# Optimization experiments

Hardware: AMD Instinct MI355X
Metric: run time of the kernel (lower is better)

Reference implementation:

```python
import jax, jax.numpy as jnp
import numpy as np

D_MODEL = 1024
N_HEADS = 16
D_HEAD = D_MODEL // N_HEADS
D_FF = 4096
B, T = 2, 2048


def layer_norm(x, gamma, beta, eps=1e-5):
    mu = jnp.mean(x, axis=-1, keepdims=True)
    var = jnp.var(x, axis=-1, keepdims=True)
    return (x - mu) * jax.lax.rsqrt(var + eps) * gamma + beta


def setup_inputs() -> dict:
    key = jax.random.key(0)
    ks = jax.random.split(key, 8)
    s = D_MODEL ** -0.5
    return {
        "x": jax.random.normal(ks[0], (B, T, D_MODEL), dtype=jnp.float32),
        "w_qkv": jax.random.normal(ks[1], (D_MODEL, 3 * D_MODEL), dtype=jnp.float32) * s,
        "w_out": jax.random.normal(ks[2], (D_MODEL, D_MODEL), dtype=jnp.float32) * s,
        "ln1_g": jnp.ones((D_MODEL,), jnp.float32),
        "ln1_b": jnp.zeros((D_MODEL,), jnp.float32),
        "ln2_g": jnp.ones((D_MODEL,), jnp.float32),
        "ln2_b": jnp.zeros((D_MODEL,), jnp.float32),
        "w1": jax.random.normal(ks[3], (D_MODEL, D_FF), dtype=jnp.float32) * s,
        "b1": jnp.zeros((D_FF,), jnp.float32),
        "w2": jax.random.normal(ks[4], (D_FF, D_MODEL), dtype=jnp.float32) * (D_FF ** -0.5),
        "b2": jnp.zeros((D_MODEL,), jnp.float32),
    }


def reference(x, w_qkv, w_out, ln1_g, ln1_b, ln2_g, ln2_b, w1, b1, w2, b2):
    Bb, Tt, C = x.shape
    h = layer_norm(x, ln1_g, ln1_b)
    qkv = h @ w_qkv  # [B,T,3C]
    q, k, v = jnp.split(qkv, 3, axis=-1)

    def heads(t):  # [B,T,C] -> [B,H,T,Dh]
        return t.reshape(Bb, Tt, N_HEADS, D_HEAD).transpose(0, 2, 1, 3)

    q, k, v = heads(q), heads(k), heads(v)
    scale = D_HEAD ** -0.5
    attn = jnp.einsum("bhqd,bhkd->bhqk", q, k) * scale
    causal = jnp.tril(jnp.ones((Tt, Tt), dtype=bool))
    attn = jnp.where(causal[None, None], attn, -jnp.inf)
    attn = jax.nn.softmax(attn, axis=-1)
    out = jnp.einsum("bhqk,bhkd->bhqd", attn, v)
    out = out.transpose(0, 2, 1, 3).reshape(Bb, Tt, C)
    x = x + out @ w_out
    h2 = layer_norm(x, ln2_g, ln2_b)
    ff = jax.nn.gelu(h2 @ w1 + b1, approximate=False) @ w2 + b2
    return x + ff
```

## Files before the change

### kernel.cpp

```cpp
#include <hip/hip_runtime.h>
#include <hip/hip_bf16.h>
#include <cstdint>

#define DM 1024
#define DFF 4096
#define NB 2
#define TT 2048
#define NH 16
#define DH 64

typedef unsigned short u16;
typedef __bf16 bf16x8 __attribute__((ext_vector_type(8)));
typedef float f32x4 __attribute__((ext_vector_type(4)));

__device__ __forceinline__ u16 f2b(float f) {
    union { float f; unsigned u; } v; v.f = f;
    unsigned u = v.u;
    return (u16)((u + 0x7FFFu + ((u >> 16) & 1u)) >> 16);
}

__device__ __forceinline__ unsigned cvtpk(float a, float b) {
    unsigned r;
    asm("v_cvt_pk_bf16_f32 %0, %1, %2" : "=v"(r) : "v"(a), "v"(b));
    return r;
}

__device__ __forceinline__ float gelu_fast(float z) {
    const float u = z * z;
    const float w = z * __builtin_fmaf(u, 0.10294324f, 2.3022082f);
    const float e = exp2f(w);
    const float r = __builtin_amdgcn_rcpf(1.0f + e);
    return z - z * r;
}

__device__ __forceinline__ f32x4 mfma_bf16(bf16x8 a, bf16x8 b, f32x4 c) {
    return __builtin_amdgcn_mfma_f32_16x16x32_bf16(a, b, c, 0, 0, 0);
}

__device__ __forceinline__ void gload_lds16(const void* g, void* l) {
    __builtin_amdgcn_global_load_lds((const __attribute__((address_space(1))) unsigned int*)g,
                                     (__attribute__((address_space(3))) unsigned int*)l, 16, 0, 0);
}

__global__ __launch_bounds__(256) void transW(const float* __restrict__ W, u16* __restrict__ Wt,
                                              int K, int N) {
    __shared__ float t[32][33];
    int tx = threadIdx.x & 31, ty = threadIdx.x >> 5;
    int k0 = blockIdx.y * 32, n0 = blockIdx.x * 32;
#pragma unroll
    for (int j = 0; j < 4; ++j)
        t[ty + 8 * j][tx] = W[(size_t)(k0 + ty + 8 * j) * N + n0 + tx];
    __syncthreads();
#pragma unroll
    for (int j = 0; j < 4; ++j)
        Wt[(size_t)(n0 + ty + 8 * j) * K + k0 + tx] = f2b(t[tx][ty + 8 * j]);
}

__global__ __launch_bounds__(256) void ln_kernel(const float* __restrict__ X,
                                                 const float* __restrict__ g,
                                                 const float* __restrict__ bt,
                                                 u16* __restrict__ H) {
    int row = blockIdx.x, tid = threadIdx.x;
    float4 v = ((const float4*)(X + (size_t)row * DM))[tid];
    float s = v.x + v.y + v.z + v.w;
    float ss = v.x * v.x + v.y * v.y + v.z * v.z + v.w * v.w;
#pragma unroll
    for (int off = 32; off >= 1; off >>= 1) {
        s += __shfl_xor(s, off);
        ss += __shfl_xor(ss, off);
    }
    __shared__ float sb[8];
    int w = tid >> 6, lane = tid & 63;
    if (lane == 0) { sb[w] = s; sb[4 + w] = ss; }
    __syncthreads();
    s = sb[0] + sb[1] + sb[2] + sb[3];
    ss = sb[4] + sb[5] + sb[6] + sb[7];
    float mu = s * (1.0f / DM);
    float var = ss * (1.0f / DM) - mu * mu;
    float rstd = rsqrtf(var + 1e-5f);
    float4 gv = ((const float4*)g)[tid];
    float4 bv = ((const float4*)bt)[tid];
    uint2 hv;
    hv.x = cvtpk((v.x - mu) * rstd * gv.x + bv.x, (v.y - mu) * rstd * gv.y + bv.y);
    hv.y = cvtpk((v.z - mu) * rstd * gv.z + bv.z, (v.w - mu) * rstd * gv.w + bv.w);
    ((uint2*)(H + (size_t)row * DM))[tid] = hv;
}

__global__ __launch_bounds__(256) void add_kernel(float* __restrict__ out,
                                                  const float* __restrict__ part, int n4) {
    int idx = blockIdx.x * 256 + threadIdx.x;
    const int stride = gridDim.x * 256;
    for (; idx < n4; idx += stride) {
        float4 a = ((const float4*)out)[idx];
        float4 p = ((const float4*)part)[idx];
        a.x += p.x; a.y += p.y; a.z += p.z; a.w += p.w;
        ((float4*)out)[idx] = a;
    }
}

template <int MODE, int DBUF, int SPLIT>
__global__ __launch_bounds__(256) void gemm_kernel(
    const u16* __restrict__ A, const u16* __restrict__ Bt, int M, int N, int K,
    u16* __restrict__ oq, u16* __restrict__ ok, u16* __restrict__ vt,
    const float* __restrict__ resid, float* __restrict__ outf,
    const float* __restrict__ bias, u16* __restrict__ outbf,
    float* __restrict__ part) {
    __shared__ __align__(16) u16 Alds[DBUF + 1][128][64];
    __shared__ __align__(16) u16 Blds[DBUF + 1][128][64];
    const int tid = threadIdx.x;
    const int lane = tid & 63;
    const int w = tid >> 6;
    const int wr = w >> 1, wc = w & 1;
    int bid = blockIdx.x + gridDim.x * blockIdx.y;
    const int nwg = gridDim.x * gridDim.y;
    bid = (bid & 7) * (nwg >> 3) + (bid >> 3);
    int mrow = bid / gridDim.x;
    int ks = 0;
    if constexpr (SPLIT) {
        const int mtiles = (nwg / gridDim.x) >> 1;
        ks = mrow >= mtiles;
        mrow -= ks * mtiles;
    }
    const int bm = mrow * 128, bn = (bid % gridDim.x) * 128;
    const int kbeg = SPLIT ? ks * (K >> 1) : 0;
    const int kend = SPLIT ? kbeg + (K >> 1) : K;
    const int l15 = lane & 15, lg = lane >> 4;
    const int srow = tid >> 3, pch = tid & 7;
    const int lc = pch ^ (srow & 7);

    f32x4 acc[4][4] = {};
    const u16* Ap = A + (size_t)(bm + srow) * K + lc * 8;
    const u16* Bp = Bt + (size_t)(bn + srow) * K + lc * 8;

#define STAGE(buf, k0)                                                          \
    {                                                                           \
        _Pragma("unroll") for (int i = 0; i < 4; ++i) {                         \
            gload_lds16(Ap + (size_t)(32 * i) * K + (k0), &Alds[buf][srow + 32 * i][pch * 8]); \
            gload_lds16(Bp + (size_t)(32 * i) * K + (k0), &Blds[buf][srow + 32 * i][pch * 8]); \
        }                                                                       \
    }

#define COMPUTE(buf)                                                            \
    {                                                                           \
        _Pragma("unroll") for (int kk = 0; kk < 2; ++kk) {                      \
            bf16x8 af[4], bfr[4];                                               \
            _Pragma("unroll") for (int f = 0; f < 4; ++f) {                     \
                const int ar = wr * 64 + f * 16 + l15;                          \
                const int br = wc * 64 + f * 16 + l15;                          \
                const int kch = kk * 4 + lg;                                    \
                af[f] = *(const bf16x8*)&Alds[buf][ar][(kch ^ (ar & 7)) * 8];   \
                bfr[f] = *(const bf16x8*)&Blds[buf][br][(kch ^ (br & 7)) * 8];  \
            }                                                                   \
            _Pragma("unroll") for (int mi = 0; mi < 4; ++mi)                    \
                _Pragma("unroll") for (int ni = 0; ni < 4; ++ni)                \
                    acc[mi][ni] = mfma_bf16(af[mi], bfr[ni], acc[mi][ni]);      \
        }                                                                       \
    }

    if constexpr (DBUF == 0) {
        for (int k0 = kbeg; k0 < kend; k0 += 64) {
            STAGE(0, k0);
            __syncthreads();
            COMPUTE(0);
            __syncthreads();
        }
    } else {
        STAGE(0, kbeg);
        for (int k0 = kbeg; k0 < kend; k0 += 64) {
            const int cur = ((k0 - kbeg) >> 6) & 1;
            if (k0 + 64 < kend) {
                STAGE(cur ^ 1, k0 + 64);
                asm volatile("s_waitcnt vmcnt(8)" ::: "memory");
            } else {
                asm volatile("s_waitcnt vmcnt(0)" ::: "memory");
            }
            __builtin_amdgcn_sched_barrier(0);
            __builtin_amdgcn_s_barrier();
            __builtin_amdgcn_sched_barrier(0);
            COMPUTE(cur);
            __builtin_amdgcn_s_barrier();
        }
    }
#undef STAGE
#undef COMPUTE

    const int m0 = bm + wr * 64, n0 = bn + wc * 64;
#pragma unroll
    for (int mi = 0; mi < 4; ++mi) {
#pragma unroll
        for (int ni = 0; ni < 4; ++ni) {
            if constexpr (MODE == 0) {
                const int n = n0 + ni * 16 + l15;
                const int which = n >> 10;
                const int hh = (n >> 6) & 15, d = n & 63;
                const int mbase = m0 + mi * 16 + 4 * lg;
                const int bb = mbase >> 11, t = mbase & 2047;
                if (which == 2) {
                    uint2 pv;
                    pv.x = cvtpk(acc[mi][ni][0], acc[mi][ni][1]);
                    pv.y = cvtpk(acc[mi][ni][2], acc[mi][ni][3]);
                    *(uint2*)(vt + (((size_t)(bb * NH + hh)) * DH + d) * TT + t) = pv;
                } else {
                    u16* dst = which == 0 ? oq : ok;
                    const float sc = which == 0 ? 0.18033688f : 1.0f;
                    const unsigned p01 = cvtpk(acc[mi][ni][0] * sc, acc[mi][ni][1] * sc);
                    const unsigned p23 = cvtpk(acc[mi][ni][2] * sc, acc[mi][ni][3] * sc);
                    u16* db = dst + (((size_t)(bb * NH + hh)) * TT + t) * DH + d;
                    db[0] = (u16)p01;
                    db[DH] = (u16)(p01 >> 16);
                    db[2 * DH] = (u16)p23;
                    db[3 * DH] = (u16)(p23 >> 16);
                }
            } else if constexpr (MODE == 2) {
                const int n = n0 + ni * 16 + l15;
                const float bn_ = bias[n];
                const float g0 = gelu_fast(acc[mi][ni][0] + bn_);
                const float g1 = gelu_fast(acc[mi][ni][1] + bn_);
                const float g2 = gelu_fast(acc[mi][ni][2] + bn_);
                const float g3 = gelu_fast(acc[mi][ni][3] + bn_);
                const unsigned p01 = cvtpk(g0, g1);
                const unsigned p23 = cvtpk(g2, g3);
                u16* db = outbf + (size_t)(m0 + mi * 16 + 4 * lg) * N + n;
                db[0] = (u16)p01;
                db[N] = (u16)(p01 >> 16);
                db[2 * N] = (u16)p23;
                db[3 * N] = (u16)(p23 >> 16);
            } else {
#pragma unroll
                for (int r = 0; r < 4; ++r) {
                    int m = m0 + mi * 16 + 4 * lg + r;
                    int n = n0 + ni * 16 + l15;
                    float v = acc[mi][ni][r];
                    size_t o = (size_t)m * N + n;
                    if constexpr (MODE == 1) {
                        outf[o] = resid[o] + v;
                    } else {
                        if (SPLIT && ks == 1)
                            part[o] = v;
                        else
                            outf[o] = resid[o] + v + bias[n];
                    }
                }
            }
        }
    }
}

__global__ __launch_bounds__(256) void attn_kernel(const u16* __restrict__ Q,
                                                   const u16* __restrict__ Kg,
                                                   const u16* __restrict__ Vtg,
                                                   u16* __restrict__ O) {
    __shared__ __align__(16) u16 Klds[4][64][64];
    __shared__ __align__(16) u16 Vlds[4][64][64];
    const int tid = threadIdx.x, lane = tid & 63, w = tid >> 6;
    const int l15 = lane & 15, lg = lane >> 4;

    int id = blockIdx.x + (blockIdx.y << 4);
    int sw = (id & 7) * 64 + (id >> 3);
    const int p = sw & 15, bh = sw >> 4;
    const size_t base = (size_t)bh * TT * DH;
    const int b = bh >> 4, hh = bh & 15;

    const int srow = tid >> 3, pch = tid & 7;
    const int lc = pch ^ (srow & 7);

    const int src0 = (((2 * lg) & 3) << 4) | l15;
    const int src1 = src0 + 16;
    const bool hi = (lg >> 1) != 0;

#define ASTAGE(buf, kv)                                                                     \
    {                                                                                       \
        gload_lds16(Kg + base + (size_t)((kv) * 64 + srow) * DH + lc * 8,                   \
                    &Klds[buf][srow][pch * 8]);                                             \
        gload_lds16(Kg + base + (size_t)((kv) * 64 + srow + 32) * DH + lc * 8,              \
                    &Klds[buf][srow + 32][pch * 8]);                                        \
        gload_lds16(Vtg + base + (size_t)srow * TT + (kv) * 64 + lc * 8,                    \
                    &Vlds[buf][srow][pch * 8]);                                             \
        gload_lds16(Vtg + base + (size_t)(srow + 32) * TT + (kv) * 64 + lc * 8,             \
                    &Vlds[buf][srow + 32][pch * 8]);                                        \
    }

    for (int half = 0; half < 2; ++half) {
        const int qt = half ? (31 - p) : p;
        const int nkv = qt + 1;
        const int qrow = qt * 64 + w * 16 + l15;
        uint4 qu0 = *(const uint4*)(Q + base + (size_t)qrow * DH + 8 * lg);
        uint4 qu1 = *(const uint4*)(Q + base + (size_t)qrow * DH + 32 + 8 * lg);
        asm volatile("" : "+v"(qu0.x), "+v"(qu0.y), "+v"(qu0.z), "+v"(qu0.w),
                          "+v"(qu1.x), "+v"(qu1.y), "+v"(qu1.z), "+v"(qu1.w));
        const bf16x8 qf0 = *(const bf16x8*)&qu0;
        const bf16x8 qf1 = *(const bf16x8*)&qu1;

        f32x4 o[4] = {};
        float lsum = 0.0f;

        auto compute_tile = [&](int buf, bool masked, int kvi) {
            f32x4 s[4] = {};
            __builtin_amdgcn_s_setprio(1);
#pragma unroll
            for (int nf = 0; nf < 4; ++nf) {
                const int row = nf * 16 + l15;
                bf16x8 kb0 = *(const bf16x8*)&Klds[buf][row][(lg ^ (l15 & 7)) * 8];
                bf16x8 kb1 = *(const bf16x8*)&Klds[buf][row][((4 + lg) ^ (l15 & 7)) * 8];
                s[nf] = mfma_bf16(kb0, qf0, s[nf]);
                s[nf] = mfma_bf16(kb1, qf1, s[nf]);
            }
            __builtin_amdgcn_s_setprio(0);

            if (masked) {
#pragma unroll
                for (int nf = 0; nf < 4; ++nf) {
                    const int tg = kvi * 64 + nf * 16 + 4 * lg;
#pragma unroll
                    for (int r = 0; r < 4; ++r)
                        if (tg + r > qrow) s[nf][r] = -1e30f;
                }
            }

            float ps = 0.0f;
#pragma unroll
            for (int nf = 0; nf < 4; ++nf) {
#pragma unroll
                for (int r = 0; r < 4; ++r) {
                    const float pp = exp2f(s[nf][r]);
                    s[nf][r] = pp;
                    ps += pp;
                }
            }
            lsum += ps;

            unsigned pk[4][2];
#pragma unroll
            for (int nf = 0; nf < 4; ++nf) {
                pk[nf][0] = cvtpk(s[nf][0], s[nf][1]);
                pk[nf][1] = cvtpk(s[nf][2], s[nf][3]);
            }
            bf16x8 pa[2];
#pragma unroll
            for (int kf = 0; kf < 2; ++kf) {
                unsigned a0 = __shfl((int)pk[2 * kf][0], src0);
                unsigned a1 = __shfl((int)pk[2 * kf][1], src0);
                unsigned a2 = __shfl((int)pk[2 * kf][0], src1);
                unsigned a3 = __shfl((int)pk[2 * kf][1], src1);
                unsigned c0 = __shfl((int)pk[2 * kf + 1][0], src0);
                unsigned c1 = __shfl((int)pk[2 * kf + 1][1], src0);
                unsigned c2 = __shfl((int)pk[2 * kf + 1][0], src1);
                unsigned c3 = __shfl((int)pk[2 * kf + 1][1], src1);
                uint4 wv;
                wv.x = hi ? c0 : a0;
                wv.y = hi ? c1 : a1;
                wv.z = hi ? c2 : a2;
                wv.w = hi ? c3 : a3;
                pa[kf] = *(const bf16x8*)&wv;
            }

            __builtin_amdgcn_s_setprio(1);
#pragma unroll
            for (int nf = 0; nf < 4; ++nf) {
                const int row = nf * 16 + l15;
                bf16x8 vb0 = *(const bf16x8*)&Vlds[buf][row][(lg ^ (l15 & 7)) * 8];
                bf16x8 vb1 = *(const bf16x8*)&Vlds[buf][row][((4 + lg) ^ (l15 & 7)) * 8];
                o[nf] = mfma_bf16(vb0, pa[0], o[nf]);
                o[nf] = mfma_bf16(vb1, pa[1], o[nf]);
            }
            __builtin_amdgcn_s_setprio(0);
        };

        ASTAGE(0, 0);
        if (nkv > 1) ASTAGE(1, 1);

        for (int kv = 0; kv < nkv; kv += 2) {
            int nst = 0;
            if (kv + 2 < nkv) { ASTAGE((kv + 2) & 3, kv + 2); nst += 4; }
            if (kv + 3 < nkv) { ASTAGE((kv + 3) & 3, kv + 3); nst += 4; }
            if (nst == 8)
                asm volatile("s_waitcnt vmcnt(8)" ::: "memory");
            else if (nst == 4)
                asm volatile("s_waitcnt vmcnt(4)" ::: "memory");
            else
                asm volatile("s_waitcnt vmcnt(0)" ::: "memory");
            __builtin_amdgcn_sched_barrier(0);
            __builtin_amdgcn_s_barrier();
            __builtin_amdgcn_sched_barrier(0);

            compute_tile(kv & 3, kv == qt, kv);
            if (kv + 1 < nkv) compute_tile((kv + 1) & 3, kv + 1 == qt, kv + 1);

            __builtin_amdgcn_s_barrier();
        }

        lsum += __shfl_xor(lsum, 16);
        lsum += __shfl_xor(lsum, 32);
        const float linv = 1.0f / lsum;
#pragma unroll
        for (int nf = 0; nf < 4; ++nf) {
            uint2 pv;
            pv.x = cvtpk(o[nf][0] * linv, o[nf][1] * linv);
            pv.y = cvtpk(o[nf][2] * linv, o[nf][3] * linv);
            *(uint2*)(O + ((size_t)b * TT + qrow) * DM + hh * DH + nf * 16 + 4 * lg) = pv;
        }
    }
#undef ASTAGE
}

extern "C" void kernel_launch(void* const* d_in, const int* in_sizes, int n_in,
                              void* d_out, int out_size, void* d_ws, size_t ws_size,
                              hipStream_t stream) {
    const float* x = (const float*)d_in[0];
    const float* wqkv = (const float*)d_in[1];
    const float* wout = (const float*)d_in[2];
    const float* ln1g = (const float*)d_in[3];
    const float* ln1b = (const float*)d_in[4];
    const float* ln2g = (const float*)d_in[5];
    const float* ln2b = (const float*)d_in[6];
    const float* w1 = (const float*)d_in[7];
    const float* b1 = (const float*)d_in[8];
    const float* w2 = (const float*)d_in[9];
    const float* b2 = (const float*)d_in[10];
    float* out = (float*)d_out;
    char* ws = (char*)d_ws;

    u16* wqkv_t = (u16*)(ws + 0);
    u16* wout_t = (u16*)(ws + 6291456);
    u16* w1_t   = (u16*)(ws + 8388608);
    u16* w2_t   = (u16*)(ws + 16777216);
    u16* h_bf   = (u16*)(ws + 25165824);
    u16* q_bf   = (u16*)(ws + 33554432);
    u16* k_bf   = (u16*)(ws + 41943040);
    u16* vt_bf  = (u16*)(ws + 50331648);
    u16* at_bf  = (u16*)(ws + 58720256);
    float* x1   = (float*)(ws + 67108864);
    u16* ff1_bf = q_bf;
    float* p1   = (float*)(ws + 0);

    transW<<<dim3(96, 32), 256, 0, stream>>>(wqkv, wqkv_t, 1024, 3072);
    transW<<<dim3(32, 32), 256, 0, stream>>>(wout, wout_t, 1024, 1024);
    transW<<<dim3(128, 32), 256, 0, stream>>>(w1, w1_t, 1024, 4096);
    transW<<<dim3(32, 128), 256, 0, stream>>>(w2, w2_t, 4096, 1024);

    ln_kernel<<<4096, 256, 0, stream>>>(x, ln1g, ln1b, h_bf);

    gemm_kernel<0, 1, 0><<<dim3(24, 32), 256, 0, stream>>>(h_bf, wqkv_t, 4096, 3072, 1024,
                                                           q_bf, k_bf, vt_bf,
                                                           nullptr, nullptr, nullptr, nullptr,
                                                           nullptr);

    attn_kernel<<<dim3(16, 32), 256, 0, stream>>>(q_bf, k_bf, vt_bf, at_bf);

    gemm_kernel<1, 1, 0><<<dim3(8, 32), 256, 0, stream>>>(at_bf, wout_t, 4096, 1024, 1024,
                                                          nullptr, nullptr, nullptr,
                                                          x, x1, nullptr, nullptr, nullptr);

    ln_kernel<<<4096, 256, 0, stream>>>(x1, ln2g, ln2b, h_bf);

    gemm_kernel<2, 1, 0><<<dim3(32, 32), 256, 0, stream>>>(h_bf, w1_t, 4096, 4096, 1024,
                                                           nullptr, nullptr, nullptr,
                                                           nullptr, nullptr, b1, ff1_bf,
                                                           nullptr);

    gemm_kernel<3, 1, 1><<<dim3(8, 64), 256, 0, stream>>>(ff1_bf, w2_t, 4096, 1024, 4096,
                                                          nullptr, nullptr, nullptr,
                                                          x1, out, b2, nullptr, p1);

    add_kernel<<<2048, 256, 0, stream>>>(out, p1, 4096 * 1024 / 4);
}
```

Before: 244.6 us.

## Add 256x256-tile 8-wave GEMM with phased prefetch for QKV and FFN1

Adds a new GEMM kernel that uses 256x256 output tiles with 512 threads (8 waves), double-buffered LDS, and an interleaved schedule: each k-tile is split into four MFMA phases, and global-to-LDS loads for the next tiles are issued between them, with setprio raised around the MFMA blocks. The QKV projection and the first FFN GEMM switch to this kernel. The larger tiles increase operand reuse and arithmetic intensity per LDS load. In exchange, fewer workgroups are launched (192 and 256), which risks leaving CUs idle or imbalanced. The heavier register and LDS use per block (128 KB of LDS) may also limit occupancy.

```diff
diff --git a/kernel.cpp b/kernel.cpp
--- a/kernel.cpp
+++ b/kernel.cpp
@@ -95,6 +95,154 @@
         float4 p = ((const float4*)part)[idx];
         a.x += p.x; a.y += p.y; a.z += p.z; a.w += p.w;
         ((float4*)out)[idx] = a;
+    }
+}
+
+template <int MODE>
+__global__ __launch_bounds__(512, 2) void gemm256(
+    const u16* __restrict__ A, const u16* __restrict__ Bt, int M, int N, int K,
+    u16* __restrict__ oq, u16* __restrict__ ok, u16* __restrict__ vt,
+    const float* __restrict__ bias, u16* __restrict__ outbf) {
+    __shared__ __align__(16) u16 Alds[2][256][64];
+    __shared__ __align__(16) u16 Blds[2][256][64];
+    const int tid = threadIdx.x;
+    const int lane = tid & 63, w = tid >> 6;
+    const int wm = w >> 2, wn = w & 3;
+    const int l15 = lane & 15, lg = lane >> 4;
+    int bid = blockIdx.x + gridDim.x * blockIdx.y;
+    const int nwg = gridDim.x * gridDim.y;
+    bid = (bid & 7) * (nwg >> 3) + (bid >> 3);
+    const int bm = (bid / gridDim.x) * 256, bn = (bid % gridDim.x) * 256;
+    const int srow = tid >> 3, pch = tid & 7;
+    const int lc = pch ^ (srow & 7);
+
+    const u16* Ap = A + (size_t)(bm + srow) * K + lc * 8;
+    const u16* Bp = Bt + (size_t)(bn + srow) * K + lc * 8;
+
+    f32x4 acc[8][4] = {};
+    bf16x8 bf[4][2];
+    const int NT = K >> 6;
+
+#define SA256(buf, t)                                                           \
+    {                                                                           \
+        _Pragma("unroll") for (int j = 0; j < 4; ++j)                           \
+            gload_lds16(Ap + (size_t)(64 * j) * K + (t) * 64,                   \
+                        &Alds[buf][srow + 64 * j][pch * 8]);                    \
+    }
+#define SB256(buf, t)                                                           \
+    {                                                                           \
+        _Pragma("unroll") for (int j = 0; j < 4; ++j)                           \
+            gload_lds16(Bp + (size_t)(64 * j) * K + (t) * 64,                   \
+                        &Blds[buf][srow + 64 * j][pch * 8]);                    \
+    }
+
+#define PHASE(BUF, P, STAGE, WAIT)                                              \
+    {                                                                           \
+        bf16x8 af[2][2];                                                        \
+        _Pragma("unroll") for (int i = 0; i < 2; ++i) {                         \
+            const int row = wm * 128 + (2 * (P) + i) * 16 + l15;                \
+            _Pragma("unroll") for (int ks = 0; ks < 2; ++ks)                    \
+                af[i][ks] =                                                     \
+                    *(const bf16x8*)&Alds[BUF][row][((ks * 4 + lg) ^ (row & 7)) * 8]; \
+        }                                                                       \
+        if constexpr ((P) == 0) {                                               \
+            _Pragma("unroll") for (int nf = 0; nf < 4; ++nf) {                  \
+                const int row = wn * 64 + nf * 16 + l15;                        \
+                _Pragma("unroll") for (int ks = 0; ks < 2; ++ks)                \
+                    bf[nf][ks] =                                                \
+                        *(const bf16x8*)&Blds[BUF][row][((ks * 4 + lg) ^ (row & 7)) * 8]; \
+            }                                                                   \
+        }                                                                       \
+        STAGE;                                                                  \
+        WAIT;                                                                   \
+        __builtin_amdgcn_s_barrier();                                           \
+        asm volatile("s_waitcnt lgkmcnt(0)" ::: "memory");                      \
+        __builtin_amdgcn_sched_barrier(0);                                      \
+        __builtin_amdgcn_s_setprio(1);                                          \
+        _Pragma("unroll") for (int i = 0; i < 2; ++i)                           \
+            _Pragma("unroll") for (int nf = 0; nf < 4; ++nf)                    \
+                _Pragma("unroll") for (int ks = 0; ks < 2; ++ks)                \
+                    acc[2 * (P) + i][nf] =                                      \
+                        mfma_bf16(af[i][ks], bf[nf][ks], acc[2 * (P) + i][nf]); \
+        __builtin_amdgcn_s_setprio(0);                                          \
+        __builtin_amdgcn_s_barrier();                                           \
+    }
+
+    SB256(0, 0);
+    SA256(0, 0);
+    SB256(1, 1);
+    asm volatile("s_waitcnt vmcnt(4)" ::: "memory");
+    __builtin_amdgcn_sched_barrier(0);
+    __builtin_amdgcn_s_barrier();
+
+    for (int it = 0; it < (NT >> 1); ++it) {
+        const int t0 = 2 * it;
+        const bool more = (t0 + 2 < NT);
+        PHASE(0, 0, { SA256(1, t0 + 1); }, {});
+        PHASE(0, 1, { if (more) SB256(0, t0 + 2); }, {});
+        PHASE(0, 2, {}, {});
+        PHASE(0, 3, {}, {
+            if (more) { asm volatile("s_waitcnt vmcnt(4)" ::: "memory"); }
+            else { asm volatile("s_waitcnt vmcnt(0)" ::: "memory"); }
+            __builtin_amdgcn_sched_barrier(0);
+        });
+        PHASE(1, 0, { if (more) SA256(0, t0 + 2); }, {});
+        PHASE(1, 1, { if (more) SB256(1, t0 + 3); }, {});
+        PHASE(1, 2, {}, {});
+        PHASE(1, 3, {}, {
+            if (more) {
+                asm volatile("s_waitcnt vmcnt(4)" ::: "memory");
+                __builtin_amdgcn_sched_barrier(0);
+            }
+        });
+    }
+#undef PHASE
+#undef SA256
+#undef SB256
+
+    const int m0 = bm + wm * 128, n0 = bn + wn * 64;
+#pragma unroll
+    for (int mi = 0; mi < 8; ++mi) {
+#pragma unroll
+        for (int ni = 0; ni < 4; ++ni) {
+            if constexpr (MODE == 0) {
+                const int n = n0 + ni * 16 + l15;
+                const int which = n >> 10;
+                const int hh = (n >> 6) & 15, d = n & 63;
+                const int mbase = m0 + mi * 16 + 4 * lg;
+                const int bb = mbase >> 11, t = mbase & 2047;
+                if (which == 2) {
+                    uint2 pv;
+                    pv.x = cvtpk(acc[mi][ni][0], acc[mi][ni][1]);
+                    pv.y = cvtpk(acc[mi][ni][2], acc[mi][ni][3]);
+                    *(uint2*)(vt + (((size_t)(bb * NH + hh)) * DH + d) * TT + t) = pv;
+                } else {
+                    u16* dst = which == 0 ? oq : ok;
+                    const float sc = which == 0 ? 0.18033688f : 1.0f;
+                    const unsigned p01 = cvtpk(acc[mi][ni][0] * sc, acc[mi][ni][1] * sc);
+                    const unsigned p23 = cvtpk(acc[mi][ni][2] * sc, acc[mi][ni][3] * sc);
+                    u16* db = dst + (((size_t)(bb * NH + hh)) * TT + t) * DH + d;
+                    db[0] = (u16)p01;
+                    db[DH] = (u16)(p01 >> 16);
+                    db[2 * DH] = (u16)p23;
+                    db[3 * DH] = (u16)(p23 >> 16);
+                }
+            } else {
+                const int n = n0 + ni * 16 + l15;
+                const float bn_ = bias[n];
+                const float g0 = gelu_fast(acc[mi][ni][0] + bn_);
+                const float g1 = gelu_fast(acc[mi][ni][1] + bn_);
+                const float g2 = gelu_fast(acc[mi][ni][2] + bn_);
+                const float g3 = gelu_fast(acc[mi][ni][3] + bn_);
+                const unsigned p01 = cvtpk(g0, g1);
+                const unsigned p23 = cvtpk(g2, g3);
+                u16* db = outbf + (size_t)(m0 + mi * 16 + 4 * lg) * N + n;
+                db[0] = (u16)p01;
+                db[N] = (u16)(p01 >> 16);
+                db[2 * N] = (u16)p23;
+                db[3 * N] = (u16)(p23 >> 16);
+            }
+        }
     }
 }
 
@@ -440,10 +588,8 @@
 
     ln_kernel<<<4096, 256, 0, stream>>>(x, ln1g, ln1b, h_bf);
 
-    gemm_kernel<0, 1, 0><<<dim3(24, 32), 256, 0, stream>>>(h_bf, wqkv_t, 4096, 3072, 1024,
-                                                           q_bf, k_bf, vt_bf,
-                                                           nullptr, nullptr, nullptr, nullptr,
-                                                           nullptr);
+    gemm256<0><<<dim3(12, 16), 512, 0, stream>>>(h_bf, wqkv_t, 4096, 3072, 1024,
+                                                 q_bf, k_bf, vt_bf, nullptr, nullptr);
 
     attn_kernel<<<dim3(16, 32), 256, 0, stream>>>(q_bf, k_bf, vt_bf, at_bf);
 
@@ -453,10 +599,8 @@
 
     ln_kernel<<<4096, 256, 0, stream>>>(x1, ln2g, ln2b, h_bf);
 
-    gemm_kernel<2, 1, 0><<<dim3(32, 32), 256, 0, stream>>>(h_bf, w1_t, 4096, 4096, 1024,
-                                                           nullptr, nullptr, nullptr,
-                                                           nullptr, nullptr, b1, ff1_bf,
-                                                           nullptr);
+    gemm256<2><<<dim3(16, 16), 512, 0, stream>>>(h_bf, w1_t, 4096, 4096, 1024,
+                                                 nullptr, nullptr, nullptr, b1, ff1_bf);
 
     gemm_kernel<3, 1, 1><<<dim3(8, 64), 256, 0, stream>>>(ff1_bf, w2_t, 4096, 1024, 4096,
                                                           nullptr, nullptr, nullptr,
```

Result: no change. 241.7 us (-1.2%).
